# Kernel tuning notes

Hardware: AMD Instinct MI355X
Metric: run time of the kernel (lower is better)

## Reference

```python
import jax, jax.numpy as jnp
import numpy as np

B, L, E, D, A = 32, 2048, 1024, 1024, 1024

def setup_inputs() -> dict:
    key = jax.random.key(0)
    k1, k2, k3, k4, k5 = jax.random.split(key, 5)
    s_e = 1.0 / np.sqrt(E)
    s_d = 1.0 / np.sqrt(D)
    s_a = 1.0 / np.sqrt(A)
    return {
        "encoder_outputs": jax.random.normal(k1, (B, L, E), dtype=jnp.float32),
        "decoder_hidden": jax.random.normal(k2, (B, D), dtype=jnp.float32),
        "mask": jnp.ones((B, L), dtype=jnp.int32),
        # nn.Linear weights are [out, in]; uniform(-1/sqrt(in), 1/sqrt(in))
        "W1": jax.random.uniform(k3, (A, E), jnp.float32, -s_e, s_e),
        "W2": jax.random.uniform(k4, (A, D), jnp.float32, -s_d, s_d),
        "v": jax.random.uniform(k5, (1, A), jnp.float32, -s_a, s_a),
    }

def reference(encoder_outputs, decoder_hidden, mask, W1, W2, v):
    # enc_t: [B,L,A], dec_t: [B,1,A]
    enc_t = jnp.einsum('ble,ae->bla', encoder_outputs, W1)
    dec_t = jnp.einsum('bd,ad->ba', decoder_hidden, W2)[:, None, :]
    combined = jnp.tanh(enc_t + dec_t)                       # [B,L,A]
    scores = jnp.einsum('bla,a->bl', combined, v[0])          # [B,L]
    scores = jnp.where(mask == 0, -jnp.inf, scores)
    attn = jax.nn.softmax(scores, axis=-1)                    # [B,L]
    context = jnp.einsum('bl,ble->be', attn, encoder_outputs) # [B,E]
    return (context, attn)
```

## Files before the change

kernel.cpp:

```cpp
#include <hip/hip_runtime.h>
#include <stdint.h>

typedef __bf16 bf16x8 __attribute__((ext_vector_type(8)));
typedef float f32x4 __attribute__((ext_vector_type(4)));
typedef unsigned short ushort8v __attribute__((ext_vector_type(8)));

__device__ __forceinline__ void gload_lds16(const void* g, void* l) {
  __builtin_amdgcn_global_load_lds(
      (const __attribute__((address_space(1))) void*)g,
      (__attribute__((address_space(3))) void*)l, 16, 0, 0);
}

__device__ __forceinline__ unsigned short f2bf(float f) {
  union { float f; unsigned int u; } x; x.f = f;
  unsigned int r = x.u + 0x7FFFu + ((x.u >> 16) & 1u);
  return (unsigned short)(r >> 16);
}

__device__ __forceinline__ float ftanh(float x) {
  float ax = fabsf(x);
  float e = __expf(-2.0f * ax);
  float r = (1.0f - e) / (1.0f + e);
  return copysignf(r, x);
}

__global__ __launch_bounds__(256) void w1cvt_kernel(
    const float* __restrict__ W1, unsigned short* __restrict__ w1b) {
  const int g = blockIdx.x * 256 + threadIdx.x;
  const int chunk = g >> 10;
  const int d16 = g & 1023;
  const int col = d16 >> 2, s = d16 & 3;
  const int np = chunk >> 5, ks = chunk & 31;
  const float* src = W1 + (size_t)(np * 256 + col) * 1024 + ks * 32 +
                     ((s ^ ((col >> 1) & 3)) * 8);
  const float4 v0 = *(const float4*)src;
  const float4 v1 = *(const float4*)(src + 4);
  ushort8v o;
  o[0] = f2bf(v0.x); o[1] = f2bf(v0.y); o[2] = f2bf(v0.z); o[3] = f2bf(v0.w);
  o[4] = f2bf(v1.x); o[5] = f2bf(v1.y); o[6] = f2bf(v1.z); o[7] = f2bf(v1.w);
  *((ushort8v*)w1b + g) = o;
}

__global__ __launch_bounds__(256) void dec_proj_kernel(
    const float* __restrict__ dec, const float* __restrict__ W2,
    float* __restrict__ u) {
  __shared__ __align__(16) float w2s[1024];
  const int a = blockIdx.x;
  const int t = threadIdx.x;
  *(float4*)(w2s + t * 4) = *(const float4*)(W2 + (size_t)a * 1024 + t * 4);
  __syncthreads();
  const int wid = t >> 6, l = t & 63;
  for (int bi = 0; bi < 8; ++bi) {
    const int b = wid * 8 + bi;
    const float* dp = dec + (size_t)b * 1024;
    float acc = 0.f;
#pragma unroll
    for (int i = 0; i < 4; ++i) {
      const int k = i * 256 + l * 4;
      const float4 dv = *(const float4*)(dp + k);
      const float4 wv = *(const float4*)(w2s + k);
      acc = fmaf(dv.x, wv.x, acc); acc = fmaf(dv.y, wv.y, acc);
      acc = fmaf(dv.z, wv.z, acc); acc = fmaf(dv.w, wv.w, acc);
    }
#pragma unroll
    for (int m = 1; m < 64; m <<= 1) acc += __shfl_xor(acc, m, 64);
    if (l == 0) u[(size_t)b * 1024 + a] = acc;
  }
}

__global__ __launch_bounds__(256, 2) void scores_kernel(
    const float* __restrict__ enc, const unsigned short* __restrict__ w1b,
    const float* __restrict__ u, const float* __restrict__ vvec,
    float* __restrict__ spart) {
  __shared__ __align__(16) char Al[16384];
  __shared__ __align__(16) char Bl[32768];
  __shared__ __align__(16) float sred[256];

  const int t = threadIdx.x;
  const int bid = blockIdx.x;
  const int np = (bid >> 3) & 3;
  const int panel = (bid & 7) + ((bid >> 5) << 3);
  const int m0 = panel * 128;
  const int n0 = np * 256;
  const int b = panel >> 4;
  const int l = t & 63, wid = t >> 6;
  const int wr = wid >> 1, wc = wid & 1;
  const int lm = l & 15, lg = l >> 4;

  const int soff = (lg ^ ((lm >> 1) & 3)) * 16;
  const int abase = (wr * 64 + lm) * 64 + soff;
  const int bbase = (wc * 128 + lm) * 64 + soff;
  const char* w1base = (const char*)w1b + (size_t)(np * 32) * 16384;
  const float* ub = u + (size_t)b * 1024;

  const int row0 = t >> 2;
  const int s0 = t & 3;
  const int xo = (s0 ^ ((row0 >> 1) & 3)) * 8;
  const float* srcA = enc + (size_t)(m0 + row0) * 1024 + xo;
  const int adst = t * 16;

  f32x4 acc[4][8];
#pragma unroll
  for (int mi = 0; mi < 4; ++mi)
#pragma unroll
    for (int ni = 0; ni < 8; ++ni) acc[mi][ni] = (f32x4){0.f, 0.f, 0.f, 0.f};

#pragma unroll
  for (int i = 0; i < 4; ++i)
    gload_lds16(w1base + i * 4096 + t * 16, Bl + i * 4096 + t * 16);
  {
    const float4 p0 = *(const float4*)srcA;
    const float4 p1 = *(const float4*)(srcA + 4);
    const float4 p2 = *(const float4*)(srcA + 65536);
    const float4 p3 = *(const float4*)(srcA + 65540);
    ushort8v o0, o1;
    o0[0] = f2bf(p0.x); o0[1] = f2bf(p0.y); o0[2] = f2bf(p0.z); o0[3] = f2bf(p0.w);
    o0[4] = f2bf(p1.x); o0[5] = f2bf(p1.y); o0[6] = f2bf(p1.z); o0[7] = f2bf(p1.w);
    o1[0] = f2bf(p2.x); o1[1] = f2bf(p2.y); o1[2] = f2bf(p2.z); o1[3] = f2bf(p2.w);
    o1[4] = f2bf(p3.x); o1[5] = f2bf(p3.y); o1[6] = f2bf(p3.z); o1[7] = f2bf(p3.w);
    *(ushort8v*)(Al + adst) = o0;
    *(ushort8v*)(Al + 4096 + adst) = o1;
  }
  __syncthreads();

#pragma unroll 2
  for (int ks = 0; ks < 32; ++ks) {
    const int abuf = (ks & 1) * 8192;
    const int bbuf = (ks & 1) * 16384;
    float4 p0, p1, p2, p3;
    if (ks < 31) {
      const char* wn = w1base + (size_t)(ks + 1) * 16384;
#pragma unroll
      for (int i = 0; i < 4; ++i)
        gload_lds16(wn + i * 4096 + t * 16,
                    Bl + (bbuf ^ 16384) + i * 4096 + t * 16);
      const float* sa = srcA + (ks + 1) * 32;
      p0 = *(const float4*)sa;
      p1 = *(const float4*)(sa + 4);
      p2 = *(const float4*)(sa + 65536);
      p3 = *(const float4*)(sa + 65540);
    }
    bf16x8 af[4], bf[8];
#pragma unroll
    for (int mi = 0; mi < 4; ++mi)
      af[mi] = *(const bf16x8*)(Al + abuf + abase + mi * 1024);
#pragma unroll
    for (int ni = 0; ni < 8; ++ni)
      bf[ni] = *(const bf16x8*)(Bl + bbuf + bbase + ni * 1024);
    __builtin_amdgcn_s_setprio(1);
#pragma unroll
    for (int mi = 0; mi < 4; ++mi)
#pragma unroll
      for (int ni = 0; ni < 8; ++ni)
        acc[mi][ni] = __builtin_amdgcn_mfma_f32_16x16x32_bf16(
            af[mi], bf[ni], acc[mi][ni], 0, 0, 0);
    __builtin_amdgcn_s_setprio(0);
    if (ks < 31) {
      ushort8v o0, o1;
      o0[0] = f2bf(p0.x); o0[1] = f2bf(p0.y); o0[2] = f2bf(p0.z); o0[3] = f2bf(p0.w);
      o0[4] = f2bf(p1.x); o0[5] = f2bf(p1.y); o0[6] = f2bf(p1.z); o0[7] = f2bf(p1.w);
      o1[0] = f2bf(p2.x); o1[1] = f2bf(p2.y); o1[2] = f2bf(p2.z); o1[3] = f2bf(p2.w);
      o1[4] = f2bf(p3.x); o1[5] = f2bf(p3.y); o1[6] = f2bf(p3.z); o1[7] = f2bf(p3.w);
      *(ushort8v*)(Al + (abuf ^ 8192) + adst) = o0;
      *(ushort8v*)(Al + (abuf ^ 8192) + 4096 + adst) = o1;
    }
    __syncthreads();
  }

  float rowp[4][4];
#pragma unroll
  for (int mi = 0; mi < 4; ++mi)
#pragma unroll
    for (int j = 0; j < 4; ++j) rowp[mi][j] = 0.f;
#pragma unroll
  for (int ni = 0; ni < 8; ++ni) {
    const int colA = n0 + wc * 128 + ni * 16 + lm;
    const float uu = ub[colA], vv = vvec[colA];
#pragma unroll
    for (int mi = 0; mi < 4; ++mi)
#pragma unroll
      for (int j = 0; j < 4; ++j)
        rowp[mi][j] += ftanh(acc[mi][ni][j] + uu) * vv;
  }
#pragma unroll
  for (int m = 1; m < 16; m <<= 1)
#pragma unroll
    for (int mi = 0; mi < 4; ++mi)
#pragma unroll
      for (int j = 0; j < 4; ++j) rowp[mi][j] += __shfl_xor(rowp[mi][j], m, 64);
  if (lm == 0) {
#pragma unroll
    for (int mi = 0; mi < 4; ++mi)
#pragma unroll
      for (int j = 0; j < 4; ++j)
        sred[wc * 128 + wr * 64 + mi * 16 + lg * 4 + j] = rowp[mi][j];
  }
  __syncthreads();
  if (t < 128) {
    spart[(size_t)np * 65536 + m0 + t] = sred[t] + sred[128 + t];
  }
}

__global__ __launch_bounds__(256) void softmax_kernel(
    const float* __restrict__ spart, float* __restrict__ out,
    const int* __restrict__ mask) {
  __shared__ float wred[4];
  const int bidx = blockIdx.x;
  const int t = threadIdx.x;
  const int r8 = bidx * 2048 + t * 8;
  float* at = out + 32768 + (size_t)bidx * 2048;
  const int* mk = mask + (size_t)bidx * 2048;
  float v[8] = {0.f, 0.f, 0.f, 0.f, 0.f, 0.f, 0.f, 0.f};
#pragma unroll
  for (int np = 0; np < 4; ++np) {
    const float4 s0 = *(const float4*)(spart + (size_t)np * 65536 + r8);
    const float4 s1 = *(const float4*)(spart + (size_t)np * 65536 + r8 + 4);
    v[0] += s0.x; v[1] += s0.y; v[2] += s0.z; v[3] += s0.w;
    v[4] += s1.x; v[5] += s1.y; v[6] += s1.z; v[7] += s1.w;
  }
  const int4 q0 = *(const int4*)(mk + t * 8);
  const int4 q1 = *(const int4*)(mk + t * 8 + 4);
  int q[8] = {q0.x, q0.y, q0.z, q0.w, q1.x, q1.y, q1.z, q1.w};
  float mx = -3.0e38f;
#pragma unroll
  for (int j = 0; j < 8; ++j) if (q[j] != 0) mx = fmaxf(mx, v[j]);
#pragma unroll
  for (int m = 1; m < 64; m <<= 1) mx = fmaxf(mx, __shfl_xor(mx, m, 64));
  if ((t & 63) == 0) wred[t >> 6] = mx;
  __syncthreads();
  mx = fmaxf(fmaxf(wred[0], wred[1]), fmaxf(wred[2], wred[3]));
  __syncthreads();
  float pp[8]; float sum = 0.f;
#pragma unroll
  for (int j = 0; j < 8; ++j) {
    pp[j] = (q[j] != 0) ? __expf(v[j] - mx) : 0.f;
    sum += pp[j];
  }
#pragma unroll
  for (int m = 1; m < 64; m <<= 1) sum += __shfl_xor(sum, m, 64);
  if ((t & 63) == 0) wred[t >> 6] = sum;
  __syncthreads();
  sum = (wred[0] + wred[1]) + (wred[2] + wred[3]);
  const float inv = 1.0f / sum;
  const float4 o0 = {pp[0] * inv, pp[1] * inv, pp[2] * inv, pp[3] * inv};
  const float4 o1 = {pp[4] * inv, pp[5] * inv, pp[6] * inv, pp[7] * inv};
  *(float4*)(at + t * 8) = o0;
  *(float4*)(at + t * 8 + 4) = o1;
}

__global__ __launch_bounds__(256) void context_kernel(
    const float* __restrict__ enc, float* __restrict__ out) {
  __shared__ __align__(16) float attnS[2048];
  __shared__ __align__(16) float red[8 * 128];
  const int bid = blockIdx.x;
  const int b = bid >> 3, ec = bid & 7;
  const int e0 = ec * 128;
  const int t = threadIdx.x;
  const float* attn = out + 32768 + (size_t)b * 2048;
#pragma unroll
  for (int i = 0; i < 8; ++i) attnS[i * 256 + t] = attn[i * 256 + t];
  __syncthreads();
  const int el = (t & 31) * 4;
  const int ls = t >> 5;
  f32x4 acc = {0.f, 0.f, 0.f, 0.f};
  const float* ebase = enc + (size_t)b * 2048 * 1024 + e0 + el;
  for (int l2 = ls; l2 < 2048; l2 += 8) {
    const float a = attnS[l2];
    const float4 ev = *(const float4*)(ebase + (size_t)l2 * 1024);
    acc[0] = fmaf(a, ev.x, acc[0]);
    acc[1] = fmaf(a, ev.y, acc[1]);
    acc[2] = fmaf(a, ev.z, acc[2]);
    acc[3] = fmaf(a, ev.w, acc[3]);
  }
  *(f32x4*)(red + ls * 128 + el) = acc;
  __syncthreads();
  if (t < 128) {
    float s = 0.f;
#pragma unroll
    for (int i = 0; i < 8; ++i) s += red[i * 128 + t];
    out[(size_t)b * 1024 + e0 + t] = s;
  }
}

extern "C" void kernel_launch(void* const* d_in, const int* in_sizes, int n_in,
                              void* d_out, int out_size, void* d_ws,
                              size_t ws_size, hipStream_t stream) {
  const float* enc = (const float*)d_in[0];
  const float* dec = (const float*)d_in[1];
  const int* mask = (const int*)d_in[2];
  const float* W1 = (const float*)d_in[3];
  const float* W2 = (const float*)d_in[4];
  const float* v = (const float*)d_in[5];
  float* out = (float*)d_out;
  char* ws = (char*)d_ws;
  unsigned short* w1b = (unsigned short*)ws;
  float* u = (float*)(ws + (2u << 20));
  float* spart = (float*)(ws + (2u << 20) + (128u << 10));

  w1cvt_kernel<<<512, 256, 0, stream>>>(W1, w1b);
  dec_proj_kernel<<<1024, 256, 0, stream>>>(dec, W2, u);
  scores_kernel<<<2048, 256, 0, stream>>>(enc, w1b, u, v, spart);
  softmax_kernel<<<32, 256, 0, stream>>>(spart, out, mask);
  context_kernel<<<256, 256, 0, stream>>>(enc, out);
}
```

Before: 275.0 us.

## Emit bf16 copy of encoder outputs in scores GEMM and read it in context

While the scores GEMM converts each fp32 encoder tile to bf16, the column-panel-0 blocks also write that bf16 tile to a workspace buffer. A new context kernel then reads the half-size bf16 copy instead of the fp32 input, cutting the context pass's memory reads. The trade-off is about 128 MB of extra writes inside the GEMM and lower precision in the context sum. The bf16 conversion also moves from a manual rounding routine to the native __bf16 cast. The new path only runs when the workspace is large enough, otherwise the old fp32 context kernel is used.

After: 312.6 us. 1.14x slower.

```diff
diff --git a/kernel.cpp b/kernel.cpp
--- a/kernel.cpp
+++ b/kernel.cpp
@@ -15,6 +15,11 @@
   union { float f; unsigned int u; } x; x.f = f;
   unsigned int r = x.u + 0x7FFFu + ((x.u >> 16) & 1u);
   return (unsigned short)(r >> 16);
+}
+
+__device__ __forceinline__ float bf2f(unsigned short h) {
+  union { unsigned int u; float f; } x; x.u = ((unsigned int)h) << 16;
+  return x.f;
 }
 
 __device__ __forceinline__ float ftanh(float x) {
@@ -22,6 +27,13 @@
   float e = __expf(-2.0f * ax);
   float r = (1.0f - e) / (1.0f + e);
   return copysignf(r, x);
+}
+
+__device__ __forceinline__ bf16x8 cvt8(float4 a, float4 b) {
+  bf16x8 o;
+  o[0] = (__bf16)a.x; o[1] = (__bf16)a.y; o[2] = (__bf16)a.z; o[3] = (__bf16)a.w;
+  o[4] = (__bf16)b.x; o[5] = (__bf16)b.y; o[6] = (__bf16)b.z; o[7] = (__bf16)b.w;
+  return o;
 }
 
 __global__ __launch_bounds__(256) void w1cvt_kernel(
@@ -71,7 +83,8 @@
 __global__ __launch_bounds__(256, 2) void scores_kernel(
     const float* __restrict__ enc, const unsigned short* __restrict__ w1b,
     const float* __restrict__ u, const float* __restrict__ vvec,
-    float* __restrict__ spart) {
+    float* __restrict__ spart, unsigned short* __restrict__ enc16,
+    const int wr16) {
   __shared__ __align__(16) char Al[16384];
   __shared__ __align__(16) char Bl[32768];
   __shared__ __align__(16) float sred[256];
@@ -79,7 +92,7 @@
   const int t = threadIdx.x;
   const int bid = blockIdx.x;
   const int np = (bid >> 3) & 3;
-  const int panel = (bid & 7) + ((bid >> 5) << 3);
+  const int panel = (bid & 7) | ((bid >> 5) << 3);
   const int m0 = panel * 128;
   const int n0 = np * 256;
   const int b = panel >> 4;
@@ -97,13 +110,17 @@
   const int s0 = t & 3;
   const int xo = (s0 ^ ((row0 >> 1) & 3)) * 8;
   const float* srcA = enc + (size_t)(m0 + row0) * 1024 + xo;
+  unsigned short* e16b = enc16 + (size_t)(m0 + row0) * 1024 + xo;
   const int adst = t * 16;
+  const bool wr0 = (wr16 != 0) && (np == 0);
 
   f32x4 acc[4][8];
 #pragma unroll
   for (int mi = 0; mi < 4; ++mi)
 #pragma unroll
     for (int ni = 0; ni < 8; ++ni) acc[mi][ni] = (f32x4){0.f, 0.f, 0.f, 0.f};
+
+  bf16x8 opend0, opend1;
 
 #pragma unroll
   for (int i = 0; i < 4; ++i)
@@ -113,28 +130,29 @@
     const float4 p1 = *(const float4*)(srcA + 4);
     const float4 p2 = *(const float4*)(srcA + 65536);
     const float4 p3 = *(const float4*)(srcA + 65540);
-    ushort8v o0, o1;
-    o0[0] = f2bf(p0.x); o0[1] = f2bf(p0.y); o0[2] = f2bf(p0.z); o0[3] = f2bf(p0.w);
-    o0[4] = f2bf(p1.x); o0[5] = f2bf(p1.y); o0[6] = f2bf(p1.z); o0[7] = f2bf(p1.w);
-    o1[0] = f2bf(p2.x); o1[1] = f2bf(p2.y); o1[2] = f2bf(p2.z); o1[3] = f2bf(p2.w);
-    o1[4] = f2bf(p3.x); o1[5] = f2bf(p3.y); o1[6] = f2bf(p3.z); o1[7] = f2bf(p3.w);
-    *(ushort8v*)(Al + adst) = o0;
-    *(ushort8v*)(Al + 4096 + adst) = o1;
+    opend0 = cvt8(p0, p1);
+    opend1 = cvt8(p2, p3);
+    *(bf16x8*)(Al + adst) = opend0;
+    *(bf16x8*)(Al + 4096 + adst) = opend1;
   }
   __syncthreads();
 
 #pragma unroll 2
-  for (int ks = 0; ks < 32; ++ks) {
-    const int abuf = (ks & 1) * 8192;
-    const int bbuf = (ks & 1) * 16384;
+  for (int kt = 0; kt < 32; ++kt) {
+    const int abuf = (kt & 1) * 8192;
+    const int bbuf = (kt & 1) * 16384;
+    if (wr0) {
+      *(bf16x8*)(e16b + kt * 32) = opend0;
+      *(bf16x8*)(e16b + 65536 + kt * 32) = opend1;
+    }
     float4 p0, p1, p2, p3;
-    if (ks < 31) {
-      const char* wn = w1base + (size_t)(ks + 1) * 16384;
+    if (kt < 31) {
+      const char* wn = w1base + (size_t)(kt + 1) * 16384;
 #pragma unroll
       for (int i = 0; i < 4; ++i)
         gload_lds16(wn + i * 4096 + t * 16,
                     Bl + (bbuf ^ 16384) + i * 4096 + t * 16);
-      const float* sa = srcA + (ks + 1) * 32;
+      const float* sa = srcA + (kt + 1) * 32;
       p0 = *(const float4*)sa;
       p1 = *(const float4*)(sa + 4);
       p2 = *(const float4*)(sa + 65536);
@@ -155,14 +173,11 @@
         acc[mi][ni] = __builtin_amdgcn_mfma_f32_16x16x32_bf16(
             af[mi], bf[ni], acc[mi][ni], 0, 0, 0);
     __builtin_amdgcn_s_setprio(0);
-    if (ks < 31) {
-      ushort8v o0, o1;
-      o0[0] = f2bf(p0.x); o0[1] = f2bf(p0.y); o0[2] = f2bf(p0.z); o0[3] = f2bf(p0.w);
-      o0[4] = f2bf(p1.x); o0[5] = f2bf(p1.y); o0[6] = f2bf(p1.z); o0[7] = f2bf(p1.w);
-      o1[0] = f2bf(p2.x); o1[1] = f2bf(p2.y); o1[2] = f2bf(p2.z); o1[3] = f2bf(p2.w);
-      o1[4] = f2bf(p3.x); o1[5] = f2bf(p3.y); o1[6] = f2bf(p3.z); o1[7] = f2bf(p3.w);
-      *(ushort8v*)(Al + (abuf ^ 8192) + adst) = o0;
-      *(ushort8v*)(Al + (abuf ^ 8192) + 4096 + adst) = o1;
+    if (kt < 31) {
+      opend0 = cvt8(p0, p1);
+      opend1 = cvt8(p2, p3);
+      *(bf16x8*)(Al + (abuf ^ 8192) + adst) = opend0;
+      *(bf16x8*)(Al + (abuf ^ 8192) + 4096 + adst) = opend1;
     }
     __syncthreads();
   }
@@ -246,6 +261,41 @@
   const float4 o1 = {pp[4] * inv, pp[5] * inv, pp[6] * inv, pp[7] * inv};
   *(float4*)(at + t * 8) = o0;
   *(float4*)(at + t * 8 + 4) = o1;
+}
+
+__global__ __launch_bounds__(256) void context16_kernel(
+    const unsigned short* __restrict__ enc16, float* __restrict__ out) {
+  __shared__ __align__(16) float attnS[2048];
+  __shared__ __align__(16) float red[16 * 132];
+  const int bid = blockIdx.x;
+  const int b = bid >> 3, ec = bid & 7;
+  const int e0 = ec * 128;
+  const int t = threadIdx.x;
+  const float* attn = out + 32768 + (size_t)b * 2048;
+#pragma unroll
+  for (int i = 0; i < 8; ++i) attnS[i * 256 + t] = attn[i * 256 + t];
+  __syncthreads();
+  const int el = (t & 15) * 8;
+  const int ls = t >> 4;
+  float acc[8];
+#pragma unroll
+  for (int j = 0; j < 8; ++j) acc[j] = 0.f;
+  const unsigned short* eb = enc16 + (size_t)b * 2048 * 1024 + e0 + el;
+  for (int l2 = ls; l2 < 2048; l2 += 16) {
+    const float a = attnS[l2];
+    const ushort8v ev = *(const ushort8v*)(eb + (size_t)l2 * 1024);
+#pragma unroll
+    for (int j = 0; j < 8; ++j) acc[j] = fmaf(a, bf2f(ev[j]), acc[j]);
+  }
+#pragma unroll
+  for (int j = 0; j < 8; ++j) red[ls * 132 + el + j] = acc[j];
+  __syncthreads();
+  if (t < 128) {
+    float s = 0.f;
+#pragma unroll
+    for (int i = 0; i < 16; ++i) s += red[i * 132 + t];
+    out[(size_t)b * 1024 + e0 + t] = s;
+  }
 }
 
 __global__ __launch_bounds__(256) void context_kernel(
@@ -294,12 +344,20 @@
   float* out = (float*)d_out;
   char* ws = (char*)d_ws;
   unsigned short* w1b = (unsigned short*)ws;
-  float* u = (float*)(ws + (2u << 20));
-  float* spart = (float*)(ws + (2u << 20) + (128u << 10));
+  float* u = (float*)(ws + 2097152);
+  float* spart = (float*)(ws + 2097152 + 131072);
+  unsigned short* enc16 =
+      (unsigned short*)(ws + 2097152 + 131072 + 1048576);
+  const size_t NEED = 2097152ull + 131072ull + 1048576ull + 134217728ull;
+  const int big = (ws_size >= NEED) ? 1 : 0;
 
   w1cvt_kernel<<<512, 256, 0, stream>>>(W1, w1b);
   dec_proj_kernel<<<1024, 256, 0, stream>>>(dec, W2, u);
-  scores_kernel<<<2048, 256, 0, stream>>>(enc, w1b, u, v, spart);
+  scores_kernel<<<2048, 256, 0, stream>>>(enc, w1b, u, v, spart, enc16, big);
   softmax_kernel<<<32, 256, 0, stream>>>(spart, out, mask);
-  context_kernel<<<256, 256, 0, stream>>>(enc, out);
-}
+  if (big) {
+    context16_kernel<<<256, 256, 0, stream>>>(enc16, out);
+  } else {
+    context_kernel<<<256, 256, 0, stream>>>(enc, out);
+  }
+}
```
